# Kernel tuning notes

Measured on AMD Instinct MI355X. Metric: run time of the kernel, lower is better.

Reference implementation:

```python
import jax, jax.numpy as jnp
import numpy as np

B, L, M, H, VN, VK = 128, 30, 10, 256, 32000, 2000
VT = VN + VK


def setup_inputs() -> dict:
    key = jax.random.key(0)
    ks = jax.random.split(key, 24)
    p = lambda k, shape: jax.random.normal(k, shape, jnp.float32) * 0.02
    eye = jnp.eye(H, dtype=jnp.float32)
    return {
        "sentence": jax.random.randint(ks[0], (B, L, 1), 0, VN),
        "keywords": jax.random.randint(ks[1], (B, M, 1), VN, VT),
        "categories": jax.random.randint(ks[2], (B, M, 1), VN, VT),
        "memory_size": jax.random.randint(ks[3], (B,), 1, M + 1),
        "use_teacher_forcing": 1,
        "emb": p(ks[4], (VT, H)),
        "W_ct": p(ks[5], (H, 5 * H)), "b_ct": jnp.zeros((H,), jnp.float32),
        "W_ih": p(ks[6], (4 * H, H)), "W_hh": p(ks[7], (4 * H, H)),
        "b_ih": jnp.zeros((4 * H,), jnp.float32), "b_hh": jnp.zeros((4 * H,), jnp.float32),
        "W_n": eye + p(ks[8], (H, H)), "W_k": eye + p(ks[9], (H, H)), "W_v": eye + p(ks[10], (H, H)),
        "W_nv": p(ks[11], (VN, H)), "b_nv": jnp.zeros((VN,), jnp.float32),
        "W_g": p(ks[12], (1, H)), "b_g": jnp.zeros((1,), jnp.float32),
        "W_hn": p(ks[13], (L, (L + 1) * H)), "b_hn": jnp.zeros((L,), jnp.float32),
        "W_hk": p(ks[14], (L, (L + 1) * H)), "b_hk": jnp.zeros((L,), jnp.float32),
        "W_hv": p(ks[15], (L, (L + 1) * H)), "b_hv": jnp.zeros((L,), jnp.float32),
        "W_mk": p(ks[16], (M, 4 * H)), "b_mk": jnp.zeros((M,), jnp.float32),
        "W_mv": p(ks[17], (M, 4 * H)), "b_mv": jnp.zeros((M,), jnp.float32),
    }


def _forward(sentence, keywords, categories, memory_size, use_teacher_forcing,
             emb, W_ct, b_ct, W_ih, W_hh, b_ih, b_hh, W_n, W_k, W_v,
             W_nv, b_nv, W_g, b_g, W_hn, b_hn, W_hk, b_hk, W_hv, b_hv,
             W_mk, b_mk, W_mv, b_mv):
    # prepare_memory: embed keyword/category ids, zero rows past memory_size
    ke = emb[keywords[:, :, 0]]      # (B,M,H)
    ve = emb[categories[:, :, 0]]    # (B,M,H)
    mask = (jnp.arange(M)[None, :] < memory_size[:, None])[..., None].astype(emb.dtype)
    key_mem = ke * mask
    val_mem = ve * mask
    ms = memory_size.astype(emb.dtype)[:, None]
    # prepare_history: initial hidden = (avg_mk + avg_mv)/2 at t=0
    init_h = (key_mem.sum(1) + val_mem.sum(1)) / (2.0 * ms)  # (B,H)
    hist0 = jnp.zeros((B, L, H), emb.dtype).at[:, 0, :].set(init_h)

    toks = sentence[:, 1:, 0].T          # (L-1, B) teacher tokens
    dis = jnp.arange(1, L)

    def step(carry, xs):
        histN, histK, histV, prev_h, prev_emb, loss = carry
        di, tok = xs

        def attn_h(hist, W, b):
            q = jnp.concatenate([prev_h, hist.reshape(B, -1)], axis=1)  # (B,(L+1)H)
            w = jnp.tanh(q @ W.T + b)                                    # (B,L)
            return jnp.einsum('bl,blh->bh', w, hist)

        cHN = attn_h(histN, W_hn, b_hn)
        cHK = attn_h(histK, W_hk, b_hk)
        cHV = attn_h(histV, W_hv, b_hv)
        cH = jnp.concatenate([cHN, cHK, cHV], axis=1)  # (B,3H)
        q_m = jnp.concatenate([prev_h, cH], axis=1)    # (B,4H)

        def attn_m(mem, W, b):
            w = jnp.tanh(q_m @ W.T + b)                # (B,M)
            return jnp.einsum('bm,bmh->bh', w, mem)

        cMK = attn_m(key_mem, W_mk, b_mk)
        cMV = attn_m(val_mem, W_mv, b_mv)
        # W_Ct_reshape(cat 5H) -> LSTM initial cell state
        c0 = jnp.concatenate([cH, cMK, cMV], axis=1) @ W_ct.T + b_ct  # (B,H)
        # single-step LSTM (torch gate order i,f,g,o)
        gates = prev_emb @ W_ih.T + b_ih + prev_h @ W_hh.T + b_hh
        gi, gf, gg, go = jnp.split(gates, 4, axis=1)
        c = jax.nn.sigmoid(gf) * c0 + jax.nn.sigmoid(gi) * jnp.tanh(gg)
        h = jax.nn.sigmoid(go) * jnp.tanh(c)           # (B,H)

        hN = h @ W_n.T
        hK = h @ W_k.T
        hV = h @ W_v.T
        histN = histN.at[:, di, :].set(hN)
        histK = histK.at[:, di, :].set(hK)
        histV = histV.at[:, di, :].set(hV)

        P_N = jax.nn.softmax(hN @ W_nv.T + b_nv, axis=1)                       # (B,VN)
        P_MK = jax.nn.softmax(jnp.einsum('bmh,bh->bm', key_mem, hK), axis=1)   # (B,M)
        P_MV = jax.nn.softmax(jnp.einsum('bmh,bh->bm', val_mem, hV), axis=1)
        P_M = 0.5 * (P_MK + P_MV)
        gt = jax.nn.sigmoid(h @ W_g.T + b_g)           # (B,1)
        P = jnp.concatenate([P_N * gt, P_M * (1.0 - gt)], axis=1)
        p_tok = jnp.take_along_axis(P, tok[:, None], axis=1)[:, 0]
        loss = loss - jnp.log(p_tok).sum()
        prev_emb = emb[tok]                            # teacher forcing
        return (histN, histK, histV, h, prev_emb, loss), gt

    carry0 = (hist0, hist0, hist0, init_h, emb[sentence[:, 0, 0]],
              jnp.zeros((), emb.dtype))
    carry, gs = jax.lax.scan(step, carry0, (dis, toks))
    loss = carry[5]
    g_history = jnp.zeros((B, L, 1), emb.dtype).at[:, 1:, :].set(
        jnp.transpose(gs, (1, 0, 2)))
    return loss, g_history


def reference(sentence, keywords, categories, memory_size, use_teacher_forcing,
              emb, W_ct, b_ct, W_ih, W_hh, b_ih, b_hh, W_n, W_k, W_v,
              W_nv, b_nv, W_g, b_g, W_hn, b_hn, W_hk, b_hk, W_hv, b_hv,
              W_mk, b_mk, W_mv, b_mv):
    return _forward(sentence, keywords, categories, memory_size, use_teacher_forcing,
                    emb, W_ct, b_ct, W_ih, W_hh, b_ih, b_hh, W_n, W_k, W_v,
                    W_nv, b_nv, W_g, b_g, W_hn, b_hn, W_hk, b_hk, W_hv, b_hv,
                    W_mk, b_mk, W_mv, b_mv)
```

## Files before the change

kernel.cpp:

```cpp
#include <hip/hip_runtime.h>
#include <math.h>

#define B_ 128
#define L_ 30
#define M_ 10
#define H_ 256
#define VN_ 32000
#define NCHK 500
#define NG 3712

typedef __bf16 bf16;
typedef bf16 bf16x8 __attribute__((ext_vector_type(8)));
typedef float f32x4 __attribute__((ext_vector_type(4)));

#define MFMA(a,b,c) __builtin_amdgcn_mfma_f32_16x16x32_bf16(a, b, c, 0, 0, 0)

__device__ __forceinline__ float rcpf(float x) { return __builtin_amdgcn_rcpf(x); }
__device__ __forceinline__ float sigf(float x) { return rcpf(1.f + __expf(-x)); }
__device__ __forceinline__ float ftanh(float x) {
  float e = __expf(2.f * x);
  return 1.f - 2.f * rcpf(e + 1.f);
}
__device__ __forceinline__ float u2lo(unsigned w) { return __builtin_bit_cast(float, w << 16); }
__device__ __forceinline__ float u2hi(unsigned w) { return __builtin_bit_cast(float, w & 0xffff0000u); }
__device__ __forceinline__ unsigned packbf2(float a, float b) {
  unsigned short lo = __builtin_bit_cast(unsigned short, (bf16)a);
  unsigned short hi = __builtin_bit_cast(unsigned short, (bf16)b);
  return (unsigned)lo | ((unsigned)hi << 16);
}

#if __has_builtin(__builtin_amdgcn_fdot2_f32_bf16)
typedef __bf16 bf16x2 __attribute__((ext_vector_type(2)));
__device__ __forceinline__ float dot2(unsigned x, unsigned w, float c) {
  return __builtin_amdgcn_fdot2_f32_bf16(__builtin_bit_cast(bf16x2, x),
                                         __builtin_bit_cast(bf16x2, w), c, false);
}
#else
__device__ __forceinline__ float dot2(unsigned x, unsigned w, float c) {
  c = fmaf(u2lo(x), u2lo(w), c);
  return fmaf(u2hi(x), u2hi(w), c);
}
#endif

__global__ __launch_bounds__(256) void k_prep(
    const float* W_ct, const float* W_hh,
    const float* W_n, const float* W_k, const float* W_v,
    const float* W_hn, const float* W_hk, const float* W_hv,
    const float* W_mk, const float* W_mv, const float* W_g,
    unsigned* W4g, unsigned* W4nkv, unsigned* W4ph, unsigned* WctP45,
    unsigned* W4m0, unsigned* W4qm, unsigned* W4da, unsigned* W4db, unsigned* WgP) {
  int stride = gridDim.x * blockDim.x;
  int base = blockIdx.x * blockDim.x + threadIdx.x;
  for (int idx = base; idx < 131072; idx += stride) {
    int s = idx & 3, tt = (idx >> 2) & 1023, i = idx >> 12;
    int n = 4*(tt >> 2) + s, k2 = (tt & 3) + 4*i;
    W4g[idx] = packbf2(W_hh[n*256 + 2*k2], W_hh[n*256 + 2*k2 + 1]);
  }
  for (int idx = base; idx < 98304; idx += stride) {
    int s = idx & 3, r2 = idx >> 2, tt = r2 % 384, i = r2 / 384;
    int n = 4*(tt >> 1) + s, k2 = (tt & 1) + 2*i;
    const float* src = (n < 256) ? W_n : (n < 512) ? W_k : W_v;
    int nn = n & 255;
    W4nkv[idx] = packbf2(src[nn*256 + 2*k2], src[nn*256 + 2*k2 + 1]);
  }
  for (int idx = base; idx < 98304; idx += stride) {
    int s = idx & 3, r2 = idx >> 2, q = r2 % 384, i = r2 / 384;
    int X = q >> 7, r = q & 127, j2 = r >> 1, kh = r & 1;
    int nl = 4*j2 + s, k2 = kh + 2*i;
    int col = X*256 + 2*k2;
    W4ph[idx] = packbf2(W_ct[nl*1280 + col], W_ct[nl*1280 + col + 1]);
  }
  for (int i = base; i < 65536; i += stride) {
    int X = i >> 15, r = i & 32767, k2 = r >> 8, n = r & 255;
    int col = 768 + X*256 + 2*k2;
    WctP45[i] = packbf2(W_ct[n*1280 + col], W_ct[n*1280 + col + 1]);
  }
  for (int idx = base; idx < 4096; idx += stride) {
    int s = idx & 3, tt = (idx >> 2) & 31, i = idx >> 7;
    int c = 4*(tt >> 2) + s, k2 = (tt & 3) + 4*i;
    float x0 = 0.f, x1 = 0.f;
    if (c < 10)              { x0 = W_mk[c*1024 + 2*k2]; x1 = W_mk[c*1024 + 2*k2 + 1]; }
    else if (c >= 16 && c < 26) { int m = c-16; x0 = W_mv[m*1024 + 2*k2]; x1 = W_mv[m*1024 + 2*k2 + 1]; }
    W4m0[idx] = packbf2(x0, x1);
  }
  for (int idx = base; idx < 12288; idx += stride) {
    int s = idx & 3, r2 = idx >> 2, q = r2 % 96, i = r2 / 96;
    int X = q >> 5, r = q & 31;
    int c = 4*(r >> 2) + s, k2 = (r & 3) + 4*i;
    int off = 256 + X*256 + 2*k2;
    float x0 = 0.f, x1 = 0.f;
    if (c < 10)              { x0 = W_mk[c*1024 + off]; x1 = W_mk[c*1024 + off + 1]; }
    else if (c >= 16 && c < 26) { int m = c-16; x0 = W_mv[m*1024 + off]; x1 = W_mv[m*1024 + off + 1]; }
    W4qm[idx] = packbf2(x0, x1);
  }
  for (int idx = base; idx < 491520; idx += stride) {
    int s = idx & 3, tt = (idx >> 2) & 127, i = (idx >> 9) & 31, d = idx >> 14;
    int c = 4*(tt >> 2) + s, k2 = (tt & 3) + 4*i;
    float x0 = 0.f, x1 = 0.f;
    if (c < 96) {
      int X = c >> 5, l = c & 31;
      if (l < 30) {
        const float* W = (X == 0) ? W_hn : (X == 1) ? W_hk : W_hv;
        x0 = W[l*7936 + d*256 + 2*k2]; x1 = W[l*7936 + d*256 + 2*k2 + 1];
      }
    }
    W4da[idx] = packbf2(x0, x1);
  }
  for (int idx = base; idx < 16384; idx += stride) {
    int s = idx & 3, tt = (idx >> 2) & 127, i = idx >> 9;
    int c = 4*(tt >> 2) + s, k2 = (tt & 3) + 4*i;
    float x0 = 0.f, x1 = 0.f;
    if (c < 96) {
      int X = c >> 5, l = c & 31;
      if (l < 30) {
        const float* W = (X == 0) ? W_hn : (X == 1) ? W_hk : W_hv;
        x0 = W[l*7936 + 2*k2]; x1 = W[l*7936 + 2*k2 + 1];
      }
    }
    W4db[idx] = packbf2(x0, x1);
  }
  for (int i = base; i < 128; i += stride) WgP[i] = packbf2(W_g[2*i], W_g[2*i+1]);
}

__global__ __launch_bounds__(256) void k_pregates(
    const int* sentence, const float* emb, const float* W_ih,
    const float* b_ih, const float* b_hh, float* prehg) {
  extern __shared__ char smp[];
  char* Al = smp;
  char* Bl = smp + 65536;
  __shared__ int tok_s[128];
  int blk = blockIdx.x;
  int gd = blk >> 3, nc = blk & 7;
  int t = threadIdx.x, wid = t >> 6, lane = t & 63;
  if (t < 128) tok_s[t] = sentence[t*L_ + gd];
  __syncthreads();
  for (int i = t; i < 128*32; i += 256) {
    int r = i >> 5, c8 = i & 31;
    const float* e = emb + (size_t)tok_s[r]*H_ + c8*8;
    float4 f0 = *(const float4*)e, f1 = *(const float4*)(e + 4);
    int4 v;
    v.x = (int)packbf2(f0.x, f0.y); v.y = (int)packbf2(f0.z, f0.w);
    v.z = (int)packbf2(f1.x, f1.y); v.w = (int)packbf2(f1.z, f1.w);
    *(int4*)(Al + ((r*512 + c8*16) ^ ((r&7)<<4))) = v;
    const float* wsrc = W_ih + (size_t)(nc*128 + r)*H_ + c8*8;
    float4 g0 = *(const float4*)wsrc, g1 = *(const float4*)(wsrc + 4);
    int4 w;
    w.x = (int)packbf2(g0.x, g0.y); w.y = (int)packbf2(g0.z, g0.w);
    w.z = (int)packbf2(g1.x, g1.y); w.w = (int)packbf2(g1.z, g1.w);
    *(int4*)(Bl + ((r*512 + c8*16) ^ ((r&7)<<4))) = w;
  }
  __syncthreads();
  f32x4 acc[2][8] = {};
  #pragma unroll 2
  for (int kk = 0; kk < 8; ++kk) {
    int kb2 = kk*64 + (lane>>4)*16;
    bf16x8 af[2], bfr[8];
    #pragma unroll
    for (int fi = 0; fi < 2; ++fi) {
      int m = wid*32 + fi*16 + (lane & 15);
      af[fi] = *(const bf16x8*)(Al + ((m*512 + kb2) ^ ((m&7)<<4)));
    }
    #pragma unroll
    for (int fj = 0; fj < 8; ++fj) {
      int n = fj*16 + (lane & 15);
      bfr[fj] = *(const bf16x8*)(Bl + ((n*512 + kb2) ^ ((n&7)<<4)));
    }
    #pragma unroll
    for (int fi = 0; fi < 2; ++fi)
      #pragma unroll
      for (int fj = 0; fj < 8; ++fj)
        acc[fi][fj] = MFMA(af[fi], bfr[fj], acc[fi][fj]);
  }
  #pragma unroll
  for (int fi = 0; fi < 2; ++fi)
    #pragma unroll
    for (int fj = 0; fj < 8; ++fj)
      #pragma unroll
      for (int r = 0; r < 4; ++r) {
        int row = wid*32 + fi*16 + (lane>>4)*4 + r;
        int col = nc*128 + fj*16 + (lane & 15);
        prehg[((size_t)gd*128 + row)*1024 + col] = acc[fi][fj][r] + b_ih[col] + b_hh[col];
      }
}

struct LoopP {
  const int *sentence, *keywords, *categories, *memsz;
  const float *emb;
  const unsigned *W4g, *W4nkv, *W4ph, *WctP45, *W4m0, *W4qm, *W4da, *W4db, *WgP;
  const float *prehg;
  const float *b_ct, *b_hn, *b_hk, *b_hv, *b_mk, *b_mv, *b_g;
  unsigned* hNb;
  unsigned* hNbT;
  float* gt_all;
  float* outg;
};

__global__ __launch_bounds__(1024) void k_loop(LoopP p) {
  extern __shared__ unsigned Su[];
  float* Sf = (float*)Su;
  const int t = threadIdx.x, b = blockIdx.x;
  enum { PH = 0, QM = 11520, P45 = 14400, MB = 16960,
         GA = 19520, HP = 20544, HV = 20672,
         SW = 21056, ACA = 21152, SWM = 21248, M0 = 21280,
         DA = 21312, DB = 21440,
         BCT = 21568, BH = 21824, BM = 21920, BG = 21952 };

  for (int i = t; i < 2560; i += 1024) {
    int X = i / 1280, r = i - X*1280, m = r >> 7, j = r & 127;
    int ms = p.memsz[b];
    int idx = (X == 0 ? p.keywords : p.categories)[b*M_ + m];
    unsigned u = 0;
    if (m < ms) {
      const float* e = p.emb + (size_t)idx*H_ + 2*j;
      u = packbf2(e[0], e[1]);
    }
    Su[MB + i] = u;
  }
  if (t < 256) Sf[BCT + t] = p.b_ct[t];
  if (t < 96) {
    int X = t >> 5, l = t & 31;
    const float* bh = (X == 0) ? p.b_hn : (X == 1) ? p.b_hk : p.b_hv;
    Sf[BH + t] = (l < 30) ? bh[l] : 0.f;
    Sf[ACA + t] = 0.f;
  }
  if (t < 32) {
    float v = 0.f;
    if (t < 10) v = p.b_mk[t];
    else if (t >= 16 && t < 26) v = p.b_mv[t - 16];
    Sf[BM + t] = v;
  }
  if (t == 0) { Sf[BG] = p.b_g[0]; p.outg[b*L_] = 0.f; }
  __syncthreads();
  if (t < 128) {
    float a0 = 0.f, a1 = 0.f;
    #pragma unroll
    for (int q = 0; q < 20; ++q) {
      unsigned u = Su[MB + q*128 + t];
      a0 += u2lo(u); a1 += u2hi(u);
    }
    float msf = (float)p.memsz[b];
    unsigned up = packbf2(a0 / (2.f * msf), a1 / (2.f * msf));
    Su[HP + t] = up;
    Su[HV + t] = up; Su[HV + 128 + t] = up; Su[HV + 256 + t] = up;
  }
  for (int q = t; q < 2560; q += 1024) {
    int X = q / 1280, r = q - X*1280, m = r >> 7, j = r & 127;
    float a0 = 0.f, a1 = 0.f;
    const uint2* wp = (const uint2*)(p.WctP45 + (X << 15)) + j;
    const unsigned* mb = Su + MB + X*1280 + m*128;
    #pragma unroll 4
    for (int k2 = 0; k2 < 128; ++k2) {
      uint2 w = wp[k2 << 7];
      unsigned u = mb[k2];
      a0 = dot2(u, w.x, a0);
      a1 = dot2(u, w.y, a1);
    }
    Su[P45 + q] = packbf2(a0, a1);
  }
  __syncthreads();

  for (int di = 1; di < L_; ++di) {
    {
      const float pre = p.prehg[(size_t)(((di-1) << 7) | b)*1024 + t];
      int kq = t & 3;
      const uint4* wr = (const uint4*)p.W4g + t;
      const unsigned* xp = Su + HP + kq;
      float p0 = 0.f, p1 = 0.f, p2 = 0.f, p3 = 0.f;
      #pragma unroll 8
      for (int i = 0; i < 32; ++i) {
        uint4 w = wr[(size_t)i << 10];
        unsigned x = xp[4*i];
        p0 = dot2(x, w.x, p0); p1 = dot2(x, w.y, p1);
        p2 = dot2(x, w.z, p2); p3 = dot2(x, w.w, p3);
      }
      p0 += __shfl_xor(p0, 1); p1 += __shfl_xor(p1, 1); p2 += __shfl_xor(p2, 1); p3 += __shfl_xor(p3, 1);
      p0 += __shfl_xor(p0, 2); p1 += __shfl_xor(p1, 2); p2 += __shfl_xor(p2, 2); p3 += __shfl_xor(p3, 2);
      float sel = (kq == 0) ? p0 : (kq == 1) ? p1 : (kq == 2) ? p2 : p3;
      Sf[GA + t] = pre + sel;
    }
    if (t < 128) {
      int kq = t & 3;
      const uint4* wr = (const uint4*)p.W4da + (size_t)di*4096 + t;
      const unsigned* xp = Su + HV + ((t >> 5) << 7) + kq;
      float p0 = 0.f, p1 = 0.f, p2 = 0.f, p3 = 0.f;
      #pragma unroll 8
      for (int i = 0; i < 32; ++i) {
        uint4 w = wr[i << 7];
        unsigned x = xp[4*i];
        p0 = dot2(x, w.x, p0); p1 = dot2(x, w.y, p1);
        p2 = dot2(x, w.z, p2); p3 = dot2(x, w.w, p3);
      }
      p0 += __shfl_xor(p0, 1); p1 += __shfl_xor(p1, 1); p2 += __shfl_xor(p2, 1); p3 += __shfl_xor(p3, 1);
      p0 += __shfl_xor(p0, 2); p1 += __shfl_xor(p1, 2); p2 += __shfl_xor(p2, 2); p3 += __shfl_xor(p3, 2);
      float sel = (kq == 0) ? p0 : (kq == 1) ? p1 : (kq == 2) ? p2 : p3;
      Sf[DA + t] = sel;
    } else if (t < 256) {
      int c = t - 128, kq = c & 3;
      const uint4* wr = (const uint4*)p.W4db + c;
      const unsigned* xp = Su + HP + kq;
      float p0 = 0.f, p1 = 0.f, p2 = 0.f, p3 = 0.f;
      #pragma unroll 8
      for (int i = 0; i < 32; ++i) {
        uint4 w = wr[i << 7];
        unsigned x = xp[4*i];
        p0 = dot2(x, w.x, p0); p1 = dot2(x, w.y, p1);
        p2 = dot2(x, w.z, p2); p3 = dot2(x, w.w, p3);
      }
      p0 += __shfl_xor(p0, 1); p1 += __shfl_xor(p1, 1); p2 += __shfl_xor(p2, 1); p3 += __shfl_xor(p3, 1);
      p0 += __shfl_xor(p0, 2); p1 += __shfl_xor(p1, 2); p2 += __shfl_xor(p2, 2); p3 += __shfl_xor(p3, 2);
      float sel = (kq == 0) ? p0 : (kq == 1) ? p1 : (kq == 2) ? p2 : p3;
      Sf[DB + c] = sel;
    } else if (t < 640) {
      int q = t - 256;
      int X = q >> 7, r = q & 127, kh = r & 1;
      const uint4* wr = (const uint4*)p.W4ph + q;
      const unsigned* xp = Su + HV + (X << 7) + kh;
      float p0 = 0.f, p1 = 0.f, p2 = 0.f, p3 = 0.f;
      #pragma unroll 8
      for (int i = 0; i < 64; ++i) {
        uint4 w = wr[i*384];
        unsigned x = xp[2*i];
        p0 = dot2(x, w.x, p0); p1 = dot2(x, w.y, p1);
        p2 = dot2(x, w.z, p2); p3 = dot2(x, w.w, p3);
      }
      p0 += __shfl_xor(p0, 1); p1 += __shfl_xor(p1, 1); p2 += __shfl_xor(p2, 1); p3 += __shfl_xor(p3, 1);
      unsigned val = kh ? packbf2(p2, p3) : packbf2(p0, p1);
      Su[PH + (X*30 + di-1)*128 + r] = val;
    } else if (t < 736) {
      int q = t - 640, X = q >> 5, r = q & 31, kq = r & 3;
      const uint4* wr = (const uint4*)p.W4qm + q;
      const unsigned* xp = Su + HV + (X << 7) + kq;
      float p0 = 0.f, p1 = 0.f, p2 = 0.f, p3 = 0.f;
      #pragma unroll 8
      for (int i = 0; i < 32; ++i) {
        uint4 w = wr[i*96];
        unsigned x = xp[4*i];
        p0 = dot2(x, w.x, p0); p1 = dot2(x, w.y, p1);
        p2 = dot2(x, w.z, p2); p3 = dot2(x, w.w, p3);
      }
      p0 += __shfl_xor(p0, 1); p1 += __shfl_xor(p1, 1); p2 += __shfl_xor(p2, 1); p3 += __shfl_xor(p3, 1);
      p0 += __shfl_xor(p0, 2); p1 += __shfl_xor(p1, 2); p2 += __shfl_xor(p2, 2); p3 += __shfl_xor(p3, 2);
      float sel = (kq == 0) ? p0 : (kq == 1) ? p1 : (kq == 2) ? p2 : p3;
      Sf[QM + (X*30 + di-1)*32 + r] = sel;
    } else if (t >= 768 && t < 800) {
      int r = t - 768, kq = r & 3;
      const uint4* wr = (const uint4*)p.W4m0 + r;
      const unsigned* xp = Su + HP + kq;
      float p0 = 0.f, p1 = 0.f, p2 = 0.f, p3 = 0.f;
      #pragma unroll 8
      for (int i = 0; i < 32; ++i) {
        uint4 w = wr[i << 5];
        unsigned x = xp[4*i];
        p0 = dot2(x, w.x, p0); p1 = dot2(x, w.y, p1);
        p2 = dot2(x, w.z, p2); p3 = dot2(x, w.w, p3);
      }
      p0 += __shfl_xor(p0, 1); p1 += __shfl_xor(p1, 1); p2 += __shfl_xor(p2, 1); p3 += __shfl_xor(p3, 1);
      p0 += __shfl_xor(p0, 2); p1 += __shfl_xor(p1, 2); p2 += __shfl_xor(p2, 2); p3 += __shfl_xor(p3, 2);
      float sel = (kq == 0) ? p0 : (kq == 1) ? p1 : (kq == 2) ? p2 : p3;
      Sf[M0 + r] = sel;
    }
    __syncthreads();
    if (t < 96) {
      float a = Sf[ACA + t] + Sf[DA + t];
      Sf[ACA + t] = a;
      Sf[SW + t] = ftanh(a + Sf[DB + t] + Sf[BH + t]);
    }
    __syncthreads();
    if (t < 32) {
      bool valid = (t < 10) || (t >= 16 && t < 26);
      if (valid) {
        float aN = 0.f, aK = 0.f, aV = 0.f;
        const float* sw0 = Sf + SW;
        const float* q0 = Sf + QM + t;
        for (int l = 0; l < di; ++l) {
          aN = fmaf(sw0[l],      q0[l*32],        aN);
          aK = fmaf(sw0[32 + l], q0[960 + l*32],  aK);
          aV = fmaf(sw0[64 + l], q0[1920 + l*32], aV);
        }
        Sf[SWM + t] = ftanh(Sf[M0 + t] + Sf[BM + t] + aN + aK + aV);
      }
    }
    __syncthreads();
    if (t < 128) {
      float a0 = Sf[BCT + 2*t], a1 = Sf[BCT + 2*t + 1];
      for (int X = 0; X < 3; ++X) {
        const float* swp = Sf + SW + X*32;
        const unsigned* php = Su + PH + X*3840 + t;
        float e0 = 0.f, e1 = 0.f, o0 = 0.f, o1 = 0.f;
        int l = 0;
        for (; l + 1 < di; l += 2) {
          float s0 = swp[l], s1 = swp[l+1];
          unsigned ua = php[l*128], ub = php[(l+1)*128];
          e0 = fmaf(s0, u2lo(ua), e0); e1 = fmaf(s0, u2hi(ua), e1);
          o0 = fmaf(s1, u2lo(ub), o0); o1 = fmaf(s1, u2hi(ub), o1);
        }
        if (l < di) {
          float s = swp[l]; unsigned u = php[l*128];
          e0 = fmaf(s, u2lo(u), e0); e1 = fmaf(s, u2hi(u), e1);
        }
        a0 += e0 + o0; a1 += e1 + o1;
      }
      {
        float p0 = 0.f, p1 = 0.f, q0 = 0.f, q1 = 0.f;
        #pragma unroll
        for (int m = 0; m < 10; ++m) {
          float sk = Sf[SWM + m], sv = Sf[SWM + 16 + m];
          unsigned uk = Su[P45 + m*128 + t], uv = Su[P45 + 1280 + m*128 + t];
          p0 = fmaf(sk, u2lo(uk), p0); p1 = fmaf(sk, u2hi(uk), p1);
          q0 = fmaf(sv, u2lo(uv), q0); q1 = fmaf(sv, u2hi(uv), q1);
        }
        a0 += p0 + q0; a1 += p1 + q1;
      }
      int n0 = 2*t;
      float gi0 = Sf[GA+n0],   gf0 = Sf[GA+256+n0], gg0 = Sf[GA+512+n0], go0 = Sf[GA+768+n0];
      float gi1 = Sf[GA+n0+1], gf1 = Sf[GA+257+n0], gg1 = Sf[GA+513+n0], go1 = Sf[GA+769+n0];
      float cc0 = sigf(gf0)*a0 + sigf(gi0)*ftanh(gg0);
      float cc1 = sigf(gf1)*a1 + sigf(gi1)*ftanh(gg1);
      float h0 = sigf(go0)*ftanh(cc0);
      float h1 = sigf(go1)*ftanh(cc1);
      Su[HP + t] = packbf2(h0, h1);
    }
    __syncthreads();
    if (t < 384) {
      int kh = t & 1;
      const uint4* wr = (const uint4*)p.W4nkv + t;
      const unsigned* xp = Su + HP + kh;
      float p0 = 0.f, p1 = 0.f, p2 = 0.f, p3 = 0.f;
      #pragma unroll 8
      for (int i = 0; i < 64; ++i) {
        uint4 w = wr[i*384];
        unsigned x = xp[2*i];
        p0 = dot2(x, w.x, p0); p1 = dot2(x, w.y, p1);
        p2 = dot2(x, w.z, p2); p3 = dot2(x, w.w, p3);
      }
      p0 += __shfl_xor(p0, 1); p1 += __shfl_xor(p1, 1); p2 += __shfl_xor(p2, 1); p3 += __shfl_xor(p3, 1);
      unsigned up = kh ? packbf2(p2, p3) : packbf2(p0, p1);
      Su[HV + t] = up;
      int X = t >> 7, j = t & 127;
      if (X == 0) {
        int tile = di - 1;
        p.hNb[(size_t)((tile << 7) | b)*128 + j] = up;
        int idx = ((((tile*4 + (b>>5))*8 + (j>>4))*64 + ((j>>2)&3)*16 + (b&15))*2 + ((b>>4)&1))*4 + (j&3);
        p.hNbT[idx] = up;
      }
    } else if (t >= 448 && t < 512) {
      int j = t - 448;
      float a = dot2(Su[HP + 2*j], p.WgP[2*j], 0.f);
      a = dot2(Su[HP + 2*j + 1], p.WgP[2*j + 1], a);
      #pragma unroll
      for (int o = 1; o < 64; o <<= 1) a += __shfl_xor(a, o);
      if (j == 0) {
        float g = sigf(a + Sf[BG]);
        p.gt_all[((di-1) << 7) | b] = g;
        p.outg[b*L_ + di] = g;
      }
    }
    __syncthreads();
  }
}

__global__ __launch_bounds__(256) void k_vocab(
    const unsigned* hNbT, const float* W_nv, const float* b_nv, float2* pmps) {
  extern __shared__ char smv[];
  int ch = blockIdx.x;
  int t = threadIdx.x, wid = t >> 6, lane = t & 63;
  int v0 = ch * 64;
  for (int i = t; i < 64*32; i += 256) {
    int r = i >> 5, c8 = i & 31;
    const float* wsrc = W_nv + (size_t)(v0 + r)*H_ + c8*8;
    float4 f0 = *(const float4*)wsrc, f1 = *(const float4*)(wsrc + 4);
    int4 v;
    v.x = (int)packbf2(f0.x, f0.y); v.y = (int)packbf2(f0.z, f0.w);
    v.z = (int)packbf2(f1.x, f1.y); v.w = (int)packbf2(f1.z, f1.w);
    *(int4*)(smv + ((r*512 + c8*16) ^ ((r&7)<<4))) = v;
  }
  float bb4[4];
  #pragma unroll
  for (int fj = 0; fj < 4; ++fj) bb4[fj] = b_nv[v0 + fj*16 + (lane & 15)];
  __syncthreads();
  bf16x8 Breg[8][4];
  #pragma unroll
  for (int kk = 0; kk < 8; ++kk) {
    int kb2 = kk*64 + (lane>>4)*16;
    #pragma unroll
    for (int fj = 0; fj < 4; ++fj) {
      int n = fj*16 + (lane & 15);
      Breg[kk][fj] = *(const bf16x8*)(smv + ((n*512 + kb2) ^ ((n&7)<<4)));
    }
  }
  const int4* At = (const int4*)hNbT;
  for (int tile = 0; tile < 29; ++tile) {
    f32x4 acc[2][4] = {};
    #pragma unroll
    for (int kk = 0; kk < 8; ++kk) {
      bf16x8 af[2];
      #pragma unroll
      for (int fi = 0; fi < 2; ++fi) {
        int4 u = At[((tile*4 + wid)*8 + kk)*128 + lane*2 + fi];
        af[fi] = __builtin_bit_cast(bf16x8, u);
      }
      #pragma unroll
      for (int fi = 0; fi < 2; ++fi)
        #pragma unroll
        for (int fj = 0; fj < 4; ++fj)
          acc[fi][fj] = MFMA(af[fi], Breg[kk][fj], acc[fi][fj]);
    }
    #pragma unroll
    for (int fi = 0; fi < 2; ++fi)
      #pragma unroll
      for (int r = 0; r < 4; ++r) {
        float mi = acc[fi][0][r] + bb4[0];
        #pragma unroll
        for (int fj = 1; fj < 4; ++fj) mi = fmaxf(mi, acc[fi][fj][r] + bb4[fj]);
        for (int o = 1; o < 16; o <<= 1) mi = fmaxf(mi, __shfl_xor(mi, o));
        float si = 0.f;
        #pragma unroll
        for (int fj = 0; fj < 4; ++fj) si += __expf(acc[fi][fj][r] + bb4[fj] - mi);
        for (int o = 1; o < 16; o <<= 1) si += __shfl_xor(si, o);
        if ((lane & 15) == 0) {
          int row = wid*32 + fi*16 + (lane>>4)*4 + r;
          pmps[(size_t)(tile*128 + row)*512 + ch] = make_float2(mi, si);
        }
      }
  }
}

__global__ __launch_bounds__(128) void k_combine(
    const float2* pmps, const unsigned* hNb, const float* W_nv, const float* b_nv,
    const float* gt_all, const int* sentence, float* loss_part) {
  __shared__ float red[128];
  int tile = blockIdx.x, bb = threadIdx.x;
  int g = tile*128 + bb;
  float M = -1e30f, Ssum = 0.f;
  const float2* pv = pmps + (size_t)g*512;
  #pragma unroll 4
  for (int c = 0; c < NCHK; ++c) {
    float2 v = pv[c];
    float M2 = fmaxf(M, v.x);
    Ssum = Ssum*__expf(M - M2) + v.y*__expf(v.x - M2);
    M = M2;
  }
  int tok = sentence[bb*L_ + tile + 1];
  float z = b_nv[tok];
  const unsigned* hu = hNb + (size_t)g*128;
  const float* wr = W_nv + (size_t)tok*H_;
  #pragma unroll 8
  for (int k = 0; k < 128; ++k) {
    unsigned w2 = hu[k];
    z += u2lo(w2)*wr[2*k] + u2hi(w2)*wr[2*k + 1];
  }
  float term = -(z - M - __logf(Ssum) + __logf(gt_all[g]));
  red[bb] = term;
  __syncthreads();
  for (int o = 64; o > 0; o >>= 1) {
    if (bb < o) red[bb] += red[bb + o];
    __syncthreads();
  }
  if (bb == 0) loss_part[tile] = red[0];
}

__global__ __launch_bounds__(64) void k_fin(const float* lp, float* out) {
  int t = threadIdx.x;
  float v = (t < 29) ? lp[t] : 0.f;
  for (int o = 1; o < 64; o <<= 1) v += __shfl_xor(v, o);
  if (t == 0) out[0] = v;
}

extern "C" void kernel_launch(void* const* d_in, const int* in_sizes, int n_in,
                              void* d_out, int out_size, void* d_ws, size_t ws_size,
                              hipStream_t stream) {
  const int* sentence  = (const int*)d_in[0];
  const int* keywords  = (const int*)d_in[1];
  const int* categories= (const int*)d_in[2];
  const int* memsz     = (const int*)d_in[3];
  const float* emb  = (const float*)d_in[5];
  const float* W_ct = (const float*)d_in[6];
  const float* b_ct = (const float*)d_in[7];
  const float* W_ih = (const float*)d_in[8];
  const float* W_hh = (const float*)d_in[9];
  const float* b_ih = (const float*)d_in[10];
  const float* b_hh = (const float*)d_in[11];
  const float* W_n  = (const float*)d_in[12];
  const float* W_k  = (const float*)d_in[13];
  const float* W_v  = (const float*)d_in[14];
  const float* W_nv = (const float*)d_in[15];
  const float* b_nv = (const float*)d_in[16];
  const float* W_g  = (const float*)d_in[17];
  const float* b_g  = (const float*)d_in[18];
  const float* W_hn = (const float*)d_in[19];
  const float* b_hn = (const float*)d_in[20];
  const float* W_hk = (const float*)d_in[21];
  const float* b_hk = (const float*)d_in[22];
  const float* W_hv = (const float*)d_in[23];
  const float* b_hv = (const float*)d_in[24];
  const float* W_mk = (const float*)d_in[25];
  const float* b_mk = (const float*)d_in[26];
  const float* W_mv = (const float*)d_in[27];
  const float* b_mv = (const float*)d_in[28];
  float* out = (float*)d_out;

  char* wsp = (char*)d_ws;
  size_t off = 0;
  auto alloc = [&](size_t bytes) -> void* {
    void* pp = wsp + off;
    off = (off + bytes + 255) & ~(size_t)255;
    return pp;
  };
  unsigned* W4g    = (unsigned*)alloc((size_t)131072*4);
  unsigned* W4nkv  = (unsigned*)alloc((size_t)98304*4);
  unsigned* W4ph   = (unsigned*)alloc((size_t)98304*4);
  unsigned* WctP45 = (unsigned*)alloc((size_t)65536*4);
  unsigned* W4m0   = (unsigned*)alloc((size_t)4096*4);
  unsigned* W4qm   = (unsigned*)alloc((size_t)12288*4);
  unsigned* W4da   = (unsigned*)alloc((size_t)491520*4);
  unsigned* W4db   = (unsigned*)alloc((size_t)16384*4);
  unsigned* WgP    = (unsigned*)alloc((size_t)128*4);
  float* prehg     = (float*)alloc((size_t)29*B_*1024*4);
  unsigned* hNb    = (unsigned*)alloc((size_t)29*B_*128*4);
  unsigned* hNbT   = (unsigned*)alloc((size_t)29*B_*128*4);
  float* gt_all    = (float*)alloc((size_t)29*B_*4);
  float2* pmps     = (float2*)alloc((size_t)NG*512*8);
  float* loss_part = (float*)alloc(29*4);

  k_prep<<<512, 256, 0, stream>>>(W_ct, W_hh, W_n, W_k, W_v,
      W_hn, W_hk, W_hv, W_mk, W_mv, W_g,
      W4g, W4nkv, W4ph, WctP45, W4m0, W4qm, W4da, W4db, WgP);
  k_pregates<<<232, 256, 131072, stream>>>(sentence, emb, W_ih, b_ih, b_hh, prehg);

  LoopP P;
  P.sentence = sentence; P.keywords = keywords; P.categories = categories; P.memsz = memsz;
  P.emb = emb;
  P.W4g = W4g; P.W4nkv = W4nkv; P.W4ph = W4ph; P.WctP45 = WctP45;
  P.W4m0 = W4m0; P.W4qm = W4qm; P.W4da = W4da; P.W4db = W4db; P.WgP = WgP;
  P.prehg = prehg;
  P.b_ct = b_ct; P.b_hn = b_hn; P.b_hk = b_hk; P.b_hv = b_hv;
  P.b_mk = b_mk; P.b_mv = b_mv; P.b_g = b_g;
  P.hNb = hNb; P.hNbT = hNbT; P.gt_all = gt_all; P.outg = out + 1;

  k_loop<<<B_, 1024, 87812, stream>>>(P);
  k_vocab<<<NCHK, 256, 32768, stream>>>(hNbT, W_nv, b_nv, pmps);
  k_combine<<<29, 128, 0, stream>>>(pmps, hNb, W_nv, b_nv, gt_all, sentence, loss_part);
  k_fin<<<1, 64, 0, stream>>>(loss_part, out);
}
```

Measured before the change: 659.5 us.

## Spread recurrent step matvecs across more threads with 4-way K splits

Repacks the W_n/W_k/W_v and W_ct history-projection weights so each output pair is computed by four threads splitting the K dimension instead of two, halving per-thread loop length. The per-step phases are rebalanced across the block: the query-memory and M0 matvecs move into the phase that computes the tanh scores, the memory-score and cell-update reductions are split across many threads with shuffle reductions, and the gate dot moves to later thread ranges. The goal is to shorten the serial latency of each of the 30 decode steps in the single-block-per-batch recurrent kernel, at the cost of more shuffles and more active threads per step.

```diff
diff --git a/kernel.cpp b/kernel.cpp
--- a/kernel.cpp
+++ b/kernel.cpp
@@ -57,16 +57,16 @@
     W4g[idx] = packbf2(W_hh[n*256 + 2*k2], W_hh[n*256 + 2*k2 + 1]);
   }
   for (int idx = base; idx < 98304; idx += stride) {
-    int s = idx & 3, r2 = idx >> 2, tt = r2 % 384, i = r2 / 384;
-    int n = 4*(tt >> 1) + s, k2 = (tt & 1) + 2*i;
+    int s = idx & 3, r2 = idx >> 2, tt = r2 % 768, i = r2 / 768;
+    int n = 4*(tt >> 2) + s, k2 = (tt & 3) + 4*i;
     const float* src = (n < 256) ? W_n : (n < 512) ? W_k : W_v;
     int nn = n & 255;
     W4nkv[idx] = packbf2(src[nn*256 + 2*k2], src[nn*256 + 2*k2 + 1]);
   }
   for (int idx = base; idx < 98304; idx += stride) {
-    int s = idx & 3, r2 = idx >> 2, q = r2 % 384, i = r2 / 384;
-    int X = q >> 7, r = q & 127, j2 = r >> 1, kh = r & 1;
-    int nl = 4*j2 + s, k2 = kh + 2*i;
+    int s = idx & 3, r2 = idx >> 2, q = r2 % 768, i = r2 / 768;
+    int X = q >> 8, rr = q & 255, ob = rr >> 2, kq = rr & 3;
+    int nl = 4*ob + s, k2 = kq + 4*i;
     int col = X*256 + 2*k2;
     W4ph[idx] = packbf2(W_ct[nl*1280 + col], W_ct[nl*1280 + col + 1]);
   }
@@ -310,24 +310,32 @@
       p0 += __shfl_xor(p0, 2); p1 += __shfl_xor(p1, 2); p2 += __shfl_xor(p2, 2); p3 += __shfl_xor(p3, 2);
       float sel = (kq == 0) ? p0 : (kq == 1) ? p1 : (kq == 2) ? p2 : p3;
       Sf[DB + c] = sel;
-    } else if (t < 640) {
+    } else {
       int q = t - 256;
-      int X = q >> 7, r = q & 127, kh = r & 1;
+      int X = q >> 8, rr = q & 255, ob = rr >> 2, kq = rr & 3;
       const uint4* wr = (const uint4*)p.W4ph + q;
-      const unsigned* xp = Su + HV + (X << 7) + kh;
+      const unsigned* xp = Su + HV + (X << 7) + kq;
       float p0 = 0.f, p1 = 0.f, p2 = 0.f, p3 = 0.f;
       #pragma unroll 8
-      for (int i = 0; i < 64; ++i) {
-        uint4 w = wr[i*384];
-        unsigned x = xp[2*i];
+      for (int i = 0; i < 32; ++i) {
+        uint4 w = wr[i*768];
+        unsigned x = xp[4*i];
         p0 = dot2(x, w.x, p0); p1 = dot2(x, w.y, p1);
         p2 = dot2(x, w.z, p2); p3 = dot2(x, w.w, p3);
       }
       p0 += __shfl_xor(p0, 1); p1 += __shfl_xor(p1, 1); p2 += __shfl_xor(p2, 1); p3 += __shfl_xor(p3, 1);
-      unsigned val = kh ? packbf2(p2, p3) : packbf2(p0, p1);
-      Su[PH + (X*30 + di-1)*128 + r] = val;
-    } else if (t < 736) {
-      int q = t - 640, X = q >> 5, r = q & 31, kq = r & 3;
+      p0 += __shfl_xor(p0, 2); p1 += __shfl_xor(p1, 2); p2 += __shfl_xor(p2, 2); p3 += __shfl_xor(p3, 2);
+      int phbase = PH + (X*30 + di-1)*128;
+      if (kq == 0)       Su[phbase + 2*ob]     = packbf2(p0, p1);
+      else if (kq == 2)  Su[phbase + 2*ob + 1] = packbf2(p2, p3);
+    }
+    __syncthreads();
+    if (t < 96) {
+      float a = Sf[ACA + t] + Sf[DA + t];
+      Sf[ACA + t] = a;
+      Sf[SW + t] = ftanh(a + Sf[DB + t] + Sf[BH + t]);
+    } else if (t >= 128 && t < 224) {
+      int q = t - 128, X = q >> 5, r = q & 31, kq = r & 3;
       const uint4* wr = (const uint4*)p.W4qm + q;
       const unsigned* xp = Su + HV + (X << 7) + kq;
       float p0 = 0.f, p1 = 0.f, p2 = 0.f, p3 = 0.f;
@@ -342,8 +350,8 @@
       p0 += __shfl_xor(p0, 2); p1 += __shfl_xor(p1, 2); p2 += __shfl_xor(p2, 2); p3 += __shfl_xor(p3, 2);
       float sel = (kq == 0) ? p0 : (kq == 1) ? p1 : (kq == 2) ? p2 : p3;
       Sf[QM + (X*30 + di-1)*32 + r] = sel;
-    } else if (t >= 768 && t < 800) {
-      int r = t - 768, kq = r & 3;
+    } else if (t >= 224 && t < 256) {
+      int r = t - 224, kq = r & 3;
       const uint4* wr = (const uint4*)p.W4m0 + r;
       const unsigned* xp = Su + HP + kq;
       float p0 = 0.f, p1 = 0.f, p2 = 0.f, p3 = 0.f;
@@ -360,91 +368,86 @@
       Sf[M0 + r] = sel;
     }
     __syncthreads();
-    if (t < 96) {
-      float a = Sf[ACA + t] + Sf[DA + t];
-      Sf[ACA + t] = a;
-      Sf[SW + t] = ftanh(a + Sf[DB + t] + Sf[BH + t]);
+    if (t < 512) {
+      int c = t >> 4, g = t & 15, X = g >> 2, lq = g & 3;
+      bool validc = (c < 10) || (c >= 16 && c < 26);
+      float a = 0.f;
+      if (X < 3 && validc) {
+        const float* swp = Sf + SW + X*32;
+        const float* qp = Sf + QM + X*960 + c;
+        for (int l = lq; l < di; l += 4) a = fmaf(swp[l], qp[l*32], a);
+      }
+      a += __shfl_xor(a, 1);
+      a += __shfl_xor(a, 2);
+      a += __shfl_xor(a, 4);
+      a += __shfl_xor(a, 8);
+      if (g == 0 && validc) Sf[SWM + c] = ftanh(Sf[M0 + c] + Sf[BM + c] + a);
     }
     __syncthreads();
-    if (t < 32) {
-      bool valid = (t < 10) || (t >= 16 && t < 26);
-      if (valid) {
-        float aN = 0.f, aK = 0.f, aV = 0.f;
-        const float* sw0 = Sf + SW;
-        const float* q0 = Sf + QM + t;
-        for (int l = 0; l < di; ++l) {
-          aN = fmaf(sw0[l],      q0[l*32],        aN);
-          aK = fmaf(sw0[32 + l], q0[960 + l*32],  aK);
-          aV = fmaf(sw0[64 + l], q0[1920 + l*32], aV);
-        }
-        Sf[SWM + t] = ftanh(Sf[M0 + t] + Sf[BM + t] + aN + aK + aV);
-      }
-    }
-    __syncthreads();
-    if (t < 128) {
-      float a0 = Sf[BCT + 2*t], a1 = Sf[BCT + 2*t + 1];
+    if (t < 512) {
+      int j = t >> 2, q = t & 3;
+      float a0 = 0.f, a1 = 0.f;
       for (int X = 0; X < 3; ++X) {
         const float* swp = Sf + SW + X*32;
-        const unsigned* php = Su + PH + X*3840 + t;
-        float e0 = 0.f, e1 = 0.f, o0 = 0.f, o1 = 0.f;
-        int l = 0;
-        for (; l + 1 < di; l += 2) {
-          float s0 = swp[l], s1 = swp[l+1];
-          unsigned ua = php[l*128], ub = php[(l+1)*128];
-          e0 = fmaf(s0, u2lo(ua), e0); e1 = fmaf(s0, u2hi(ua), e1);
-          o0 = fmaf(s1, u2lo(ub), o0); o1 = fmaf(s1, u2hi(ub), o1);
+        const unsigned* php = Su + PH + X*3840 + j;
+        for (int l = q; l < di; l += 4) {
+          float s = swp[l];
+          unsigned u = php[l*128];
+          a0 = fmaf(s, u2lo(u), a0);
+          a1 = fmaf(s, u2hi(u), a1);
         }
-        if (l < di) {
-          float s = swp[l]; unsigned u = php[l*128];
-          e0 = fmaf(s, u2lo(u), e0); e1 = fmaf(s, u2hi(u), e1);
-        }
-        a0 += e0 + o0; a1 += e1 + o1;
-      }
-      {
-        float p0 = 0.f, p1 = 0.f, q0 = 0.f, q1 = 0.f;
+      }
+      a0 += __shfl_xor(a0, 1); a1 += __shfl_xor(a1, 1);
+      a0 += __shfl_xor(a0, 2); a1 += __shfl_xor(a1, 2);
+      if (q == 0) {
+        a0 += Sf[BCT + 2*j]; a1 += Sf[BCT + 2*j + 1];
+        float pp0 = 0.f, pp1 = 0.f, qq0 = 0.f, qq1 = 0.f;
         #pragma unroll
         for (int m = 0; m < 10; ++m) {
           float sk = Sf[SWM + m], sv = Sf[SWM + 16 + m];
-          unsigned uk = Su[P45 + m*128 + t], uv = Su[P45 + 1280 + m*128 + t];
-          p0 = fmaf(sk, u2lo(uk), p0); p1 = fmaf(sk, u2hi(uk), p1);
-          q0 = fmaf(sv, u2lo(uv), q0); q1 = fmaf(sv, u2hi(uv), q1);
+          unsigned uk = Su[P45 + m*128 + j], uv = Su[P45 + 1280 + m*128 + j];
+          pp0 = fmaf(sk, u2lo(uk), pp0); pp1 = fmaf(sk, u2hi(uk), pp1);
+          qq0 = fmaf(sv, u2lo(uv), qq0); qq1 = fmaf(sv, u2hi(uv), qq1);
         }
-        a0 += p0 + q0; a1 += p1 + q1;
-      }
-      int n0 = 2*t;
-      float gi0 = Sf[GA+n0],   gf0 = Sf[GA+256+n0], gg0 = Sf[GA+512+n0], go0 = Sf[GA+768+n0];
-      float gi1 = Sf[GA+n0+1], gf1 = Sf[GA+257+n0], gg1 = Sf[GA+513+n0], go1 = Sf[GA+769+n0];
-      float cc0 = sigf(gf0)*a0 + sigf(gi0)*ftanh(gg0);
-      float cc1 = sigf(gf1)*a1 + sigf(gi1)*ftanh(gg1);
-      float h0 = sigf(go0)*ftanh(cc0);
-      float h1 = sigf(go1)*ftanh(cc1);
-      Su[HP + t] = packbf2(h0, h1);
+        a0 += pp0 + qq0; a1 += pp1 + qq1;
+        int n0 = 2*j;
+        float gi0 = Sf[GA+n0],   gf0 = Sf[GA+256+n0], gg0 = Sf[GA+512+n0], go0 = Sf[GA+768+n0];
+        float gi1 = Sf[GA+n0+1], gf1 = Sf[GA+257+n0], gg1 = Sf[GA+513+n0], go1 = Sf[GA+769+n0];
+        float cc0 = sigf(gf0)*a0 + sigf(gi0)*ftanh(gg0);
+        float cc1 = sigf(gf1)*a1 + sigf(gi1)*ftanh(gg1);
+        float h0 = sigf(go0)*ftanh(cc0);
+        float h1 = sigf(go1)*ftanh(cc1);
+        Su[HP + j] = packbf2(h0, h1);
+      }
     }
     __syncthreads();
-    if (t < 384) {
-      int kh = t & 1;
+    if (t < 768) {
+      int ob = t >> 2, kq = t & 3;
       const uint4* wr = (const uint4*)p.W4nkv + t;
-      const unsigned* xp = Su + HP + kh;
+      const unsigned* xp = Su + HP + kq;
       float p0 = 0.f, p1 = 0.f, p2 = 0.f, p3 = 0.f;
       #pragma unroll 8
-      for (int i = 0; i < 64; ++i) {
-        uint4 w = wr[i*384];
-        unsigned x = xp[2*i];
+      for (int i = 0; i < 32; ++i) {
+        uint4 w = wr[i*768];
+        unsigned x = xp[4*i];
         p0 = dot2(x, w.x, p0); p1 = dot2(x, w.y, p1);
         p2 = dot2(x, w.z, p2); p3 = dot2(x, w.w, p3);
       }
       p0 += __shfl_xor(p0, 1); p1 += __shfl_xor(p1, 1); p2 += __shfl_xor(p2, 1); p3 += __shfl_xor(p3, 1);
-      unsigned up = kh ? packbf2(p2, p3) : packbf2(p0, p1);
-      Su[HV + t] = up;
-      int X = t >> 7, j = t & 127;
-      if (X == 0) {
-        int tile = di - 1;
-        p.hNb[(size_t)((tile << 7) | b)*128 + j] = up;
-        int idx = ((((tile*4 + (b>>5))*8 + (j>>4))*64 + ((j>>2)&3)*16 + (b&15))*2 + ((b>>4)&1))*4 + (j&3);
-        p.hNbT[idx] = up;
-      }
-    } else if (t >= 448 && t < 512) {
-      int j = t - 448;
+      p0 += __shfl_xor(p0, 2); p1 += __shfl_xor(p1, 2); p2 += __shfl_xor(p2, 2); p3 += __shfl_xor(p3, 2);
+      if ((kq & 1) == 0) {
+        int thv = 2*ob + (kq >> 1);
+        unsigned up = (kq == 0) ? packbf2(p0, p1) : packbf2(p2, p3);
+        Su[HV + thv] = up;
+        if (thv < 128) {
+          int tile = di - 1;
+          p.hNb[(size_t)((tile << 7) | b)*128 + thv] = up;
+          int idx = ((((tile*4 + (b>>5))*8 + (thv>>4))*64 + ((thv>>2)&3)*16 + (b&15))*2 + ((b>>4)&1))*4 + (thv&3);
+          p.hNbT[idx] = up;
+        }
+      }
+    } else if (t >= 768 && t < 832) {
+      int j = t - 768;
       float a = dot2(Su[HP + 2*j], p.WgP[2*j], 0.f);
       a = dot2(Su[HP + 2*j + 1], p.WgP[2*j + 1], a);
       #pragma unroll
```

Measured after the change: 966.9 us. 46.6% more time.
